# Kernel optimization log

Hardware: AMD Instinct MI355X
Metric: run time of the kernel (lower is better)

Reference implementation:

```python
import jax, jax.numpy as jnp
import numpy as np

B, C_IN, H, W = 16, 3, 128, 128
HID = 256      # backbone hidden channels
NC = 21        # num_classes (CRF tag set)
DN = ('NCHW', 'OIHW', 'NCHW')


def setup_inputs() -> dict:
    key = jax.random.key(0)
    ks = jax.random.split(key, 6)
    return {
        "x": jax.random.normal(ks[0], (B, C_IN, H, W), jnp.float32),
        "conv1_w": jax.random.normal(ks[1], (HID, C_IN, 3, 3), jnp.float32) * 0.05,
        "conv1_b": jnp.zeros((HID,), jnp.float32),
        "conv2_w": jax.random.normal(ks[2], (NC, HID, 1, 1), jnp.float32) * 0.05,
        "conv2_b": jnp.zeros((NC,), jnp.float32),
        "start_trans": jax.random.normal(ks[3], (NC,), jnp.float32) * 0.1,
        "end_trans": jax.random.normal(ks[4], (NC,), jnp.float32) * 0.1,
        "trans": jax.random.normal(ks[5], (NC, NC), jnp.float32) * 0.1,
    }


def _backbone(x, w1, b1, w2, b2):
    h = jax.lax.conv_general_dilated(x, w1, (1, 1), 'SAME', dimension_numbers=DN)
    h = jax.nn.relu(h + b1[None, :, None, None])
    out = jax.lax.conv_general_dilated(h, w2, (1, 1), 'SAME', dimension_numbers=DN)
    return out + b2[None, :, None, None]   # [b, NC, H, W]


def _viterbi_decode(emissions, start, end, trans):
    # emissions: [b, L, C]; mask is all-True (as in the module).
    # Forward max-sum recursion (torchcrf _viterbi_decode semantics).
    score0 = emissions[:, 0] + start            # [b, C]

    def fwd(score, emit_t):
        # score[b, prev] + trans[prev, next] + emit_t[b, next] -> [b, prev, next]
        nxt = score[:, :, None] + trans[None, :, :] + emit_t[:, None, :]
        idx = jnp.argmax(nxt, axis=1).astype(jnp.int32)   # backpointers [b, C]
        return jnp.max(nxt, axis=1), idx

    emits = jnp.swapaxes(emissions[:, 1:], 0, 1)          # [L-1, b, C]
    score, hist = jax.lax.scan(fwd, score0, emits)        # hist: [L-1, b, C]
    score = score + end
    last_tag = jnp.argmax(score, axis=1).astype(jnp.int32)  # [b]

    # Backtrack: tag_t = hist[t][b, tag_{t+1}], t = L-2 .. 0
    def bwd(tag_next, idx_t):
        tag_t = jnp.take_along_axis(idx_t, tag_next[:, None], axis=1)[:, 0]
        return tag_t, tag_t

    _, tags_head = jax.lax.scan(bwd, last_tag, hist, reverse=True)  # [L-1, b]
    tags = jnp.concatenate([tags_head, last_tag[None, :]], axis=0)  # [L, b]
    return jnp.swapaxes(tags, 0, 1)                                  # [b, L]


def reference(x, conv1_w, conv1_b, conv2_w, conv2_b, start_trans, end_trans, trans):
    feats = _backbone(x, conv1_w, conv1_b, conv2_w, conv2_b)  # [b, NC, h, w]
    b, c, h, w = feats.shape
    emissions = feats.reshape(b, c, h * w).transpose(0, 2, 1)  # [b, L, C]
    tags = _viterbi_decode(emissions, start_trans, end_trans, trans)  # [b, L]
    return tags.reshape(b, h, w)
```

## Files before the change

### kernel.cpp

```cpp
#include <hip/hip_runtime.h>
#include <stdint.h>

#define NB 16
#define HH 128
#define WW 128
#define L (HH*WW)
#define CIN 3
#define HID 256
#define NC 21
#define CHUNK 256
#define NCHUNKS (L/CHUNK)
#define T_PER 32
#define NPACK (L/4)

__global__ __launch_bounds__(256) void k_conv(
    const float* __restrict__ x, const float* __restrict__ w1,
    const float* __restrict__ b1, const float* __restrict__ w2,
    const float* __restrict__ b2, float* __restrict__ emT)
{
    __shared__ float xs[CIN*4*WW];
    int tid = threadIdx.x;
    int g  = blockIdx.x * 256 + tid;
    int b  = g >> 14;
    int t0 = (blockIdx.x * 256) & (L-1);
    int y0 = t0 >> 7;
    int dy = tid >> 7;
    int xx = tid & (WW-1);
    int t  = t0 + tid;

    const float* xb = x + (size_t)b * CIN * L;
    for (int i = tid; i < CIN*4*WW; i += 256) {
        int ic  = i >> 9;
        int rem = i & 511;
        int rr  = rem >> 7;
        int cc  = rem & 127;
        int row = y0 - 1 + rr;
        xs[i] = (row >= 0 && row < HH) ? xb[ic*L + (row<<7) + cc] : 0.f;
    }
    __syncthreads();

    double p[27];
    #pragma unroll
    for (int ic = 0; ic < CIN; ++ic) {
        #pragma unroll
        for (int ky = 0; ky < 3; ++ky) {
            #pragma unroll
            for (int kx = 0; kx < 3; ++kx) {
                int xc = xx + kx - 1;
                float v = (xc >= 0 && xc < WW) ? xs[ic*512 + (dy+ky)*128 + xc] : 0.f;
                p[ic*9 + ky*3 + kx] = (double)v;
            }
        }
    }

    double acc[NC];
    #pragma unroll
    for (int c = 0; c < NC; ++c) acc[c] = 0.0;

    #pragma unroll 2
    for (int oc = 0; oc < HID; ++oc) {
        double hv = 0.0;
        #pragma unroll
        for (int j = 0; j < 27; ++j) hv += (double)w1[oc*27 + j] * p[j];
        float h32 = (float)hv;
        h32 = h32 + b1[oc];
        h32 = fmaxf(h32, 0.f);
        double hd = (double)h32;
        #pragma unroll
        for (int c = 0; c < NC; ++c) acc[c] += (double)w2[c*HID + oc] * hd;
    }
    float* dstb = emT + (size_t)b * NC * L;
    #pragma unroll
    for (int c = 0; c < NC; ++c) {
        float e32 = (float)acc[c];
        dstb[(size_t)c * L + t] = e32 + b2[c];
    }
}

#define NEGINF (-__builtin_huge_valf())
typedef int iv2 __attribute__((ext_vector_type(2)));

__global__ __launch_bounds__(64) void k_scores(
    const float* __restrict__ emT, const float* __restrict__ start,
    const float* __restrict__ endt, const float* __restrict__ trans,
    float* __restrict__ sc, int* __restrict__ last_tag)
{
    __shared__ float smem[256];
    __shared__ float fin[NC];
    int l = threadIdx.x;
    int b = blockIdx.x;
    int u = l & 31;
    int h = l >> 5;
    int n = u < NC ? u : NC-1;
    int wb = 12*h;

    int woff_dump = 64 + l;
    bool writer = (h == 0) && (u < NC);

    const float4* er4 = (const float4*)(emT + ((size_t)b * NC + n) * L);
    float*        scp = sc + (size_t)b * NC * L;

    float tcv[12];
    #pragma unroll
    for (int i = 0; i < 12; ++i) {
        int p = wb + i;
        tcv[i] = (p < NC) ? trans[p*NC + n] : NEGINF;
    }
    #pragma unroll
    for (int i = 0; i < 12; ++i) asm volatile("" : "+v"(tcv[i]));

    #define STEP(CUR, NXT, EV, OUT) { \
        float4 ra  = *(const float4*)&smem[(CUR)*128 + wb]; \
        float4 rb4 = *(const float4*)&smem[(CUR)*128 + wb + 4]; \
        float4 rc4 = *(const float4*)&smem[(CUR)*128 + wb + 8]; \
        float w0 = ra.x  + tcv[0], w1 = ra.y  + tcv[1], w2  = ra.z  + tcv[2],  w3  = ra.w  + tcv[3]; \
        float w4 = rb4.x + tcv[4], w5 = rb4.y + tcv[5], w6  = rb4.z + tcv[6],  w7  = rb4.w + tcv[7]; \
        float w8 = rc4.x + tcv[8], w9 = rc4.y + tcv[9], w10 = rc4.z + tcv[10], w11 = rc4.w + tcv[11]; \
        float m0 = fmaxf(fmaxf(w0, w1), w2); \
        float m1 = fmaxf(fmaxf(w3, w4), w5); \
        float m2 = fmaxf(fmaxf(w6, w7), w8); \
        float m3 = fmaxf(fmaxf(w9, w10), w11); \
        float qh = fmaxf(fmaxf(m0, m1), fmaxf(m2, m3)) + (EV);    \
        iv2 rr = __builtin_amdgcn_permlane32_swap(__float_as_int(qh), __float_as_int(qh), false, false); \
        float sn = fmaxf(__int_as_float(rr[0]), __int_as_float(rr[1]));   \
        smem[writer ? ((NXT)*128 + u) : woff_dump] = sn; \
        OUT = sn; }

    float4 ebuf0 = er4[0];
    float4 ebuf1 = er4[1];

    float v0 = ebuf0.x + start[n];
    smem[l]       = (l < NC) ? v0 : NEGINF;
    smem[128 + l] = NEGINF;
    float q0 = v0, q1, q2, q3;
    {
        float4 ev = ebuf0;
        ebuf0 = er4[2];
        STEP(0, 1, ev.y, q1)
        STEP(1, 0, ev.z, q2)
        STEP(0, 1, ev.w, q3)
        if (l < NC) *(float4*)(scp + n*4) = make_float4(q0, q1, q2, q3);
    }

    for (int k = 1; k < NPACK; ++k) {
        float4 ev = (k & 1) ? ebuf1 : ebuf0;
        int kp = k + 2; if (kp > NPACK-1) kp = NPACK-1;
        if (k & 1) ebuf1 = er4[kp]; else ebuf0 = er4[kp];

        STEP(1, 0, ev.x, q0)
        STEP(0, 1, ev.y, q1)
        STEP(1, 0, ev.z, q2)
        STEP(0, 1, ev.w, q3)
        if (l < NC) *(float4*)(scp + k*84 + n*4) = make_float4(q0, q1, q2, q3);
    }
    #undef STEP

    if (l < NC) fin[n] = q3;
    __syncthreads();
    if (l == 0) {
        float bv = fin[0] + endt[0]; int bt = 0;
        #pragma unroll
        for (int j = 1; j < NC; ++j) {
            float v = fin[j] + endt[j];
            if (v > bv) { bv = v; bt = j; }
        }
        last_tag[b] = bt;
    }
}

__global__ __launch_bounds__(256) void k_bp(
    const float* __restrict__ emT, const float* __restrict__ sc,
    const float* __restrict__ trans, uint8_t* __restrict__ bp)
{
    int wave = threadIdx.x >> 6;
    int lane = threadIdx.x & 63;
    int ne   = lane < NC ? lane : NC-1;

    int bidx  = blockIdx.x;
    int b     = bidx >> 7;
    int tbase = (bidx & 127) * (4*T_PER) + wave*T_PER;

    const float* emb = emT + (size_t)b * NC * L;
    const float* scp = sc  + (size_t)b * NC * L;
    uint8_t*     bpb = bp  + (size_t)b * L * NC;

    float tc[NC];
    #pragma unroll
    for (int pp = 0; pp < NC; ++pp) tc[pp] = trans[pp*NC + ne];

    for (int t = tbase; t < tbase + T_PER; ++t) {
        if (t == 0) continue;
        float target = scp[(t>>2)*84 + ne*4 + (t&3)];
        float e      = emb[(size_t)ne * L + t];
        const float* sp = scp + ((t-1)>>2)*84 + ((t-1)&3);
        int fi = 0;
        #pragma unroll
        for (int pp = NC-1; pp >= 0; --pp) {
            float cand = (sp[pp*4] + tc[pp]) + e;
            if (cand == target) fi = pp;
        }
        if (lane < NC) bpb[(size_t)t * NC + ne] = (uint8_t)fi;
    }
}

__global__ __launch_bounds__(64) void k_jump(
    const uint8_t* __restrict__ bp, uint8_t* __restrict__ J)
{
    __shared__ uint32_t lds4[CHUNK*NC/4];
    __shared__ uint8_t  segJ[8*NC];
    int l   = threadIdx.x;
    int bid = blockIdx.x;
    int b   = bid / (NCHUNKS-1);
    int k   = bid % (NCHUNKS-1) + 1;
    int cs  = k * CHUNK;

    const uint32_t* src = (const uint32_t*)(bp + (size_t)b * L * NC + (size_t)cs * NC);
    for (int i = l; i < CHUNK*NC/4; i += 64) lds4[i] = src[i];
    __syncthreads();
    const uint8_t* lb = (const uint8_t*)lds4;

    int c0 = l, c1 = l + 63, c2 = l + 126;
    bool v2 = (c2 < 8*NC);
    int t0 = c0 % NC, t1 = c1 % NC, t2 = v2 ? (c2 % NC) : 0;
    int r0 = (c0 / NC) * 32, r1 = (c1 / NC) * 32, r2 = v2 ? (c2 / NC) * 32 : 0;
    for (int i = 31; i >= 0; --i) {
        t0 = lb[(r0+i)*NC + t0];
        t1 = lb[(r1+i)*NC + t1];
        if (v2) t2 = lb[(r2+i)*NC + t2];
    }
    segJ[c0] = (uint8_t)t0;
    segJ[c1] = (uint8_t)t1;
    if (v2) segJ[c2] = (uint8_t)t2;
    __syncthreads();

    if (l < NC) {
        int tag = l;
        #pragma unroll
        for (int s = 7; s >= 0; --s) tag = segJ[s*NC + tag];
        J[((size_t)b * NCHUNKS + k) * NC + l] = (uint8_t)tag;
    }
}

__global__ __launch_bounds__(64) void k_seq(
    const uint8_t* __restrict__ J, const int* __restrict__ last_tag,
    uint8_t* __restrict__ ent)
{
    __shared__ uint32_t ldsJ4[NB*NCHUNKS*NC/4];
    int l = threadIdx.x;
    const uint32_t* src = (const uint32_t*)J;
    for (int i = l; i < NB*NCHUNKS*NC/4; i += 64) ldsJ4[i] = src[i];
    __syncthreads();
    const uint8_t* lj = (const uint8_t*)ldsJ4;

    if (l < NB) {
        int b = l;
        int tag = last_tag[b];
        ent[b * NCHUNKS + 63] = (uint8_t)tag;
        for (int k = NCHUNKS-1; k >= 1; --k) {
            tag = lj[((size_t)b * NCHUNKS + k) * NC + tag];
            ent[b * NCHUNKS + (k-1)] = (uint8_t)tag;
        }
    }
}

__global__ __launch_bounds__(64) void k_out(
    const uint8_t* __restrict__ bp, const uint8_t* __restrict__ ent,
    int* __restrict__ out)
{
    __shared__ uint32_t lds4[CHUNK*NC/4];
    __shared__ uint8_t  segJ[8*NC];
    __shared__ uint8_t  E[8];
    __shared__ int      tags[CHUNK];
    int l   = threadIdx.x;
    int bid = blockIdx.x;
    int b   = bid >> 6;
    int k   = bid & (NCHUNKS-1);
    int cs  = k * CHUNK;

    const uint32_t* src = (const uint32_t*)(bp + (size_t)b * L * NC + (size_t)cs * NC);
    for (int i = l; i < CHUNK*NC/4; i += 64) lds4[i] = src[i];
    __syncthreads();
    const uint8_t* lb = (const uint8_t*)lds4;

    int c0 = l, c1 = l + 63, c2 = l + 126;
    bool v2 = (c2 < 8*NC);
    int t0 = c0 % NC, t1 = c1 % NC, t2 = v2 ? (c2 % NC) : 0;
    int r0 = (c0 / NC) * 32, r1 = (c1 / NC) * 32, r2 = v2 ? (c2 / NC) * 32 : 0;
    for (int i = 31; i >= 0; --i) {
        t0 = lb[(r0+i)*NC + t0];
        t1 = lb[(r1+i)*NC + t1];
        if (v2) t2 = lb[(r2+i)*NC + t2];
    }
    segJ[c0] = (uint8_t)(t0 & 31);
    segJ[c1] = (uint8_t)(t1 & 31);
    if (v2) segJ[c2] = (uint8_t)(t2 & 31);
    __syncthreads();

    if (l == 0) {
        int tag = ent[b * NCHUNKS + k];
        E[7] = (uint8_t)tag;
        #pragma unroll
        for (int s = 7; s >= 1; --s) { tag = segJ[s*NC + tag]; E[s-1] = (uint8_t)tag; }
    }
    __syncthreads();

    if (l < 8) {
        int tag = E[l];
        int rb  = l * 32;
        for (int i = 31; i >= 0; --i) {
            tags[rb + i] = tag;
            tag = lb[(rb+i)*NC + tag];
        }
    }
    __syncthreads();

    int4* ob = (int4*)(out + (size_t)b * L + cs);
    ob[l] = ((const int4*)tags)[l];
}

extern "C" void kernel_launch(void* const* d_in, const int* in_sizes, int n_in,
                              void* d_out, int out_size, void* d_ws, size_t ws_size,
                              hipStream_t stream) {
    const float* x  = (const float*)d_in[0];
    const float* w1 = (const float*)d_in[1];
    const float* b1 = (const float*)d_in[2];
    const float* w2 = (const float*)d_in[3];
    const float* b2 = (const float*)d_in[4];
    const float* st = (const float*)d_in[5];
    const float* en = (const float*)d_in[6];
    const float* tr = (const float*)d_in[7];
    int* out = (int*)d_out;

    char* ws = (char*)d_ws;
    float*   em = (float*)ws;
    float*   sc = (float*)(ws + (size_t)NB*L*NC*4);
    uint8_t* bp = (uint8_t*)(ws + (size_t)NB*L*NC*8);
    int*     lt = (int*)(ws + (size_t)NB*L*NC*9);
    uint8_t* J   = (uint8_t*)ws;
    uint8_t* ent = (uint8_t*)ws + 21504;

    k_conv  <<<dim3(NB*L/256),       dim3(256), 0, stream>>>(x, w1, b1, w2, b2, em);
    k_scores<<<dim3(NB),             dim3(64),  0, stream>>>(em, st, en, tr, sc, lt);
    k_bp    <<<dim3(NB*128),         dim3(256), 0, stream>>>(em, sc, tr, bp);
    k_jump  <<<dim3(NB*(NCHUNKS-1)), dim3(64),  0, stream>>>(bp, J);
    k_seq   <<<dim3(1),              dim3(64),  0, stream>>>(J, lt, ent);
    k_out   <<<dim3(NB*NCHUNKS),     dim3(64),  0, stream>>>(bp, ent, out);
}
```

Baseline: 2.315 ms.

## Process four batch chains per wave in Viterbi score recursion

The serial forward max-sum kernel previously used one 64-lane wave per batch, with each half-wave handling 12 of the 21 predecessors and a permlane32 swap to combine them. It now runs four independent batch chains per wave: each half-wave owns two chains, and each lane reduces over all 21 predecessors itself, so no cross-lane swap is needed. This gives more independent instructions per step to hide LDS and ALU latency, but launches only 4 blocks and makes each step do more work per lane.

```diff
diff --git a/kernel.cpp b/kernel.cpp
--- a/kernel.cpp
+++ b/kernel.cpp
@@ -77,94 +77,126 @@
     }
 }
 
-#define NEGINF (-__builtin_huge_valf())
-typedef int iv2 __attribute__((ext_vector_type(2)));
-
 __global__ __launch_bounds__(64) void k_scores(
     const float* __restrict__ emT, const float* __restrict__ start,
     const float* __restrict__ endt, const float* __restrict__ trans,
     float* __restrict__ sc, int* __restrict__ last_tag)
 {
     __shared__ float smem[256];
-    __shared__ float fin[NC];
-    int l = threadIdx.x;
-    int b = blockIdx.x;
-    int u = l & 31;
-    int h = l >> 5;
-    int n = u < NC ? u : NC-1;
-    int wb = 12*h;
-
-    int woff_dump = 64 + l;
-    bool writer = (h == 0) && (u < NC);
-
-    const float4* er4 = (const float4*)(emT + ((size_t)b * NC + n) * L);
-    float*        scp = sc + (size_t)b * NC * L;
-
-    float tcv[12];
-    #pragma unroll
-    for (int i = 0; i < 12; ++i) {
-        int p = wb + i;
-        tcv[i] = (p < NC) ? trans[p*NC + n] : NEGINF;
-    }
-    #pragma unroll
-    for (int i = 0; i < 12; ++i) asm volatile("" : "+v"(tcv[i]));
-
-    #define STEP(CUR, NXT, EV, OUT) { \
-        float4 ra  = *(const float4*)&smem[(CUR)*128 + wb]; \
-        float4 rb4 = *(const float4*)&smem[(CUR)*128 + wb + 4]; \
-        float4 rc4 = *(const float4*)&smem[(CUR)*128 + wb + 8]; \
-        float w0 = ra.x  + tcv[0], w1 = ra.y  + tcv[1], w2  = ra.z  + tcv[2],  w3  = ra.w  + tcv[3]; \
-        float w4 = rb4.x + tcv[4], w5 = rb4.y + tcv[5], w6  = rb4.z + tcv[6],  w7  = rb4.w + tcv[7]; \
-        float w8 = rc4.x + tcv[8], w9 = rc4.y + tcv[9], w10 = rc4.z + tcv[10], w11 = rc4.w + tcv[11]; \
-        float m0 = fmaxf(fmaxf(w0, w1), w2); \
-        float m1 = fmaxf(fmaxf(w3, w4), w5); \
-        float m2 = fmaxf(fmaxf(w6, w7), w8); \
-        float m3 = fmaxf(fmaxf(w9, w10), w11); \
-        float qh = fmaxf(fmaxf(m0, m1), fmaxf(m2, m3)) + (EV);    \
-        iv2 rr = __builtin_amdgcn_permlane32_swap(__float_as_int(qh), __float_as_int(qh), false, false); \
-        float sn = fmaxf(__int_as_float(rr[0]), __int_as_float(rr[1]));   \
-        smem[writer ? ((NXT)*128 + u) : woff_dump] = sn; \
-        OUT = sn; }
-
-    float4 ebuf0 = er4[0];
-    float4 ebuf1 = er4[1];
-
-    float v0 = ebuf0.x + start[n];
-    smem[l]       = (l < NC) ? v0 : NEGINF;
-    smem[128 + l] = NEGINF;
-    float q0 = v0, q1, q2, q3;
+    __shared__ float fin[4*NC];
+    int l   = threadIdx.x;
+    int u   = l & 31;
+    int hi  = l >> 5;
+    int n   = u < NC ? u : NC-1;
+    int blk = blockIdx.x;
+
+    int b0 = 4*blk + hi;
+    int b1 = 4*blk + 2 + hi;
+    int cb0 = hi * 48;
+    int cb1 = (2 + hi) * 48;
+
+    bool st = (u < NC);
+    int ws0p0 = st ? (cb0 + u)      : (192 + l);
+    int ws0p1 = st ? (cb0 + 24 + u) : (192 + l);
+    int ws1p0 = st ? (cb1 + u)      : (192 + l);
+    int ws1p1 = st ? (cb1 + 24 + u) : (192 + l);
+
+    const float4* er0 = (const float4*)(emT + ((size_t)b0 * NC + n) * L);
+    const float4* er1 = (const float4*)(emT + ((size_t)b1 * NC + n) * L);
+    float* scp0 = sc + (size_t)b0 * NC * L;
+    float* scp1 = sc + (size_t)b1 * NC * L;
+
+    float tc[NC];
+    #pragma unroll
+    for (int p = 0; p < NC; ++p) tc[p] = trans[p*NC + n];
+    #pragma unroll
+    for (int p = 0; p < NC; ++p) asm volatile("" : "+v"(tc[p]));
+
+    #define COL(R0,R1,R2,R3,R4,R5, EV, WSL, OUT) { \
+        float w0  = R0.x + tc[0],  w1  = R0.y + tc[1],  w2  = R0.z + tc[2],  w3  = R0.w + tc[3]; \
+        float w4  = R1.x + tc[4],  w5  = R1.y + tc[5],  w6  = R1.z + tc[6],  w7  = R1.w + tc[7]; \
+        float w8  = R2.x + tc[8],  w9  = R2.y + tc[9],  w10 = R2.z + tc[10], w11 = R2.w + tc[11]; \
+        float w12 = R3.x + tc[12], w13 = R3.y + tc[13], w14 = R3.z + tc[14], w15 = R3.w + tc[15]; \
+        float w16 = R4.x + tc[16], w17 = R4.y + tc[17], w18 = R4.z + tc[18], w19 = R4.w + tc[19]; \
+        float w20 = R5.x + tc[20];                        \
+        float m0 = fmaxf(fmaxf(w0,  w1),  w2); \
+        float m1 = fmaxf(fmaxf(w3,  w4),  w5); \
+        float m2 = fmaxf(fmaxf(w6,  w7),  w8); \
+        float m3 = fmaxf(fmaxf(w9,  w10), w11); \
+        float m4 = fmaxf(fmaxf(w12, w13), w14); \
+        float m5 = fmaxf(fmaxf(w15, w16), w17); \
+        float m6 = fmaxf(fmaxf(w18, w19), w20); \
+        float z0 = fmaxf(fmaxf(m0, m1), m2); \
+        float z1 = fmaxf(fmaxf(m3, m4), m5); \
+        float qv = fmaxf(fmaxf(z0, z1), m6) + (EV);       \
+        smem[WSL] = qv; \
+        OUT = qv; }
+
+    #define STEPPAIR(PPR, PPW, EV0, EV1, O0, O1) { \
+        const float* pa_ = &smem[cb0 + (PPR)*24]; \
+        const float* pb_ = &smem[cb1 + (PPR)*24]; \
+        float4 A0 = *(const float4*)(pa_+0),  A1 = *(const float4*)(pa_+4),  A2 = *(const float4*)(pa_+8); \
+        float4 A3 = *(const float4*)(pa_+12), A4 = *(const float4*)(pa_+16), A5 = *(const float4*)(pa_+20); \
+        float4 B0 = *(const float4*)(pb_+0),  B1 = *(const float4*)(pb_+4),  B2 = *(const float4*)(pb_+8); \
+        float4 B3 = *(const float4*)(pb_+12), B4 = *(const float4*)(pb_+16), B5 = *(const float4*)(pb_+20); \
+        COL(A0,A1,A2,A3,A4,A5, EV0, (PPW) ? ws0p1 : ws0p0, O0) \
+        COL(B0,B1,B2,B3,B4,B5, EV1, (PPW) ? ws1p1 : ws1p0, O1) \
+    }
+
+    float4 e0a = er0[0], e0b = er0[1];
+    float4 e1a = er1[0], e1b = er1[1];
+
+    float q00, q01, q02, q03, q10, q11, q12, q13;
+
+    q00 = e0a.x + start[n];
+    q10 = e1a.x + start[n];
+    smem[ws0p0] = q00;
+    smem[ws1p0] = q10;
     {
-        float4 ev = ebuf0;
-        ebuf0 = er4[2];
-        STEP(0, 1, ev.y, q1)
-        STEP(1, 0, ev.z, q2)
-        STEP(0, 1, ev.w, q3)
-        if (l < NC) *(float4*)(scp + n*4) = make_float4(q0, q1, q2, q3);
+        float4 e0 = e0a, e1 = e1a;
+        e0a = er0[2]; e1a = er1[2];
+        STEPPAIR(0, 1, e0.y, e1.y, q01, q11)
+        STEPPAIR(1, 0, e0.z, e1.z, q02, q12)
+        STEPPAIR(0, 1, e0.w, e1.w, q03, q13)
+        if (st) {
+            *(float4*)(scp0 + n*4) = make_float4(q00, q01, q02, q03);
+            *(float4*)(scp1 + n*4) = make_float4(q10, q11, q12, q13);
+        }
     }
 
     for (int k = 1; k < NPACK; ++k) {
-        float4 ev = (k & 1) ? ebuf1 : ebuf0;
+        float4 e0 = (k & 1) ? e0b : e0a;
+        float4 e1 = (k & 1) ? e1b : e1a;
         int kp = k + 2; if (kp > NPACK-1) kp = NPACK-1;
-        if (k & 1) ebuf1 = er4[kp]; else ebuf0 = er4[kp];
-
-        STEP(1, 0, ev.x, q0)
-        STEP(0, 1, ev.y, q1)
-        STEP(1, 0, ev.z, q2)
-        STEP(0, 1, ev.w, q3)
-        if (l < NC) *(float4*)(scp + k*84 + n*4) = make_float4(q0, q1, q2, q3);
-    }
-    #undef STEP
-
-    if (l < NC) fin[n] = q3;
-    __syncthreads();
-    if (l == 0) {
-        float bv = fin[0] + endt[0]; int bt = 0;
+        if (k & 1) { e0b = er0[kp]; e1b = er1[kp]; }
+        else       { e0a = er0[kp]; e1a = er1[kp]; }
+
+        STEPPAIR(1, 0, e0.x, e1.x, q00, q10)
+        STEPPAIR(0, 1, e0.y, e1.y, q01, q11)
+        STEPPAIR(1, 0, e0.z, e1.z, q02, q12)
+        STEPPAIR(0, 1, e0.w, e1.w, q03, q13)
+        if (st) {
+            *(float4*)(scp0 + k*84 + n*4) = make_float4(q00, q01, q02, q03);
+            *(float4*)(scp1 + k*84 + n*4) = make_float4(q10, q11, q12, q13);
+        }
+    }
+    #undef STEPPAIR
+    #undef COL
+
+    if (st) {
+        fin[hi*NC + n]     = q03;
+        fin[(2+hi)*NC + n] = q13;
+    }
+    __syncthreads();
+    if (l < 4) {
+        int c = l;
+        float bv = fin[c*NC + 0] + endt[0]; int bt = 0;
         #pragma unroll
         for (int j = 1; j < NC; ++j) {
-            float v = fin[j] + endt[j];
+            float v = fin[c*NC + j] + endt[j];
             if (v > bv) { bv = v; bt = j; }
         }
-        last_tag[b] = bt;
+        last_tag[4*blk + c] = bt;
     }
 }
 
@@ -340,7 +372,7 @@
     uint8_t* ent = (uint8_t*)ws + 21504;
 
     k_conv  <<<dim3(NB*L/256),       dim3(256), 0, stream>>>(x, w1, b1, w2, b2, em);
-    k_scores<<<dim3(NB),             dim3(64),  0, stream>>>(em, st, en, tr, sc, lt);
+    k_scores<<<dim3(NB/4),           dim3(64),  0, stream>>>(em, st, en, tr, sc, lt);
     k_bp    <<<dim3(NB*128),         dim3(256), 0, stream>>>(em, sc, tr, bp);
     k_jump  <<<dim3(NB*(NCHUNKS-1)), dim3(64),  0, stream>>>(bp, J);
     k_seq   <<<dim3(1),              dim3(64),  0, stream>>>(J, lt, ent);
```

Measured after the change: 4.233 ms. 82.8% more time.
